# Kernel tuning notes

Measured on AMD Instinct MI355X. Metric: run time of the kernel, lower is better.

## Reference

```python
import jax, jax.numpy as jnp
import numpy as np
import math

D_MODEL = 256


def make_pe(h, w, d):
    # dh channels encode row index, dh channels encode column index,
    # each as interleaved sin/cos with log-spaced frequencies.
    dh = d // 2
    freqs = jnp.exp(jnp.arange(0, dh, 2, dtype=jnp.float32) * (-math.log(10000.0) / dh))  # [dh/2]
    r = jnp.arange(h, dtype=jnp.float32)[:, None] * freqs[None, :]  # [h, dh/2]
    c = jnp.arange(w, dtype=jnp.float32)[:, None] * freqs[None, :]  # [w, dh/2]
    rr = jnp.stack([jnp.sin(r), jnp.cos(r)], axis=-1).reshape(h, dh)  # interleave sin/cos
    cc = jnp.stack([jnp.sin(c), jnp.cos(c)], axis=-1).reshape(w, dh)
    pe = jnp.concatenate([
        jnp.broadcast_to(rr[:, None, :], (h, w, dh)),
        jnp.broadcast_to(cc[None, :, :], (h, w, dh)),
    ], axis=-1)  # [h, w, d]
    return pe.reshape(1, h * w, d)


def setup_inputs() -> dict:
    key = jax.random.key(0)
    h, w = 128, 128
    b = 8
    x = jax.random.normal(key, (b, h * w, D_MODEL), dtype=jnp.float32)
    return {"x": x, "h": h, "w": w}


def reference(x, h, w):
    # Dropout is identity in eval mode; the core op is PE-table generation + add.
    b, l, d = x.shape
    pe = make_pe(h, w, d)  # [1, h*w, d]
    return x + pe[:, :l]
```

## Files before the change

### kernel.cpp

```cpp
#include <hip/hip_runtime.h>
#include <math.h>


typedef float f32x4 __attribute__((ext_vector_type(4)));

__global__ __launch_bounds__(256) void pe_add_kernel(
    const float* __restrict__ x,
    const int* __restrict__ hp,
    const int* __restrict__ wp,
    float* __restrict__ out,
    unsigned int n4)
{
    unsigned int idx = blockIdx.x * blockDim.x + threadIdx.x;
    if (idx >= n4) return;

    const unsigned int ww = (unsigned int)(*wp);
    const unsigned int hh = (unsigned int)(*hp);
    const unsigned int L  = hh * ww;

    const unsigned int j = idx & 63u;
    const unsigned int t = idx >> 6;

    unsigned int l, row, col;
    if (((ww & (ww - 1u)) | (L & (L - 1u))) == 0u) {
        const unsigned int wshift = (unsigned int)__builtin_ctz(ww);
        l   = t & (L - 1u);
        row = l >> wshift;
        col = l & (ww - 1u);
    } else {
        l   = t % L;
        row = l / ww;
        col = l - row * ww;
    }

    const unsigned int d0 = j << 2;
    const unsigned int dd = d0 & 127u;
    const float pos = (float)((d0 < 128u) ? row : col);

    const unsigned int m0 = dd >> 1;
    const float cstep = 0.14391156831212787f;
    const float f0 = __expf(-(float)m0 * cstep);
    const float f1 = __expf(-(float)(m0 + 1u) * cstep);

    float s0, c0, s1, c1;
    __sincosf(pos * f0, &s0, &c0);
    __sincosf(pos * f1, &s1, &c1);

    const f32x4 xv = reinterpret_cast<const f32x4*>(x)[idx];
    const f32x4 pe = { s0, c0, s1, c1 };
    const f32x4 ov = xv + pe;
    __builtin_nontemporal_store(ov, reinterpret_cast<f32x4*>(out) + idx);
}

extern "C" void kernel_launch(void* const* d_in, const int* in_sizes, int n_in,
                              void* d_out, int out_size, void* d_ws, size_t ws_size,
                              hipStream_t stream) {
    const float* x = (const float*)d_in[0];
    const int* hp  = (const int*)d_in[1];
    const int* wp  = (const int*)d_in[2];
    float* out     = (float*)d_out;

    const unsigned int n4 = (unsigned int)(out_size / 4);
    const unsigned int blocks = (n4 + 255u) / 256u;
    pe_add_kernel<<<blocks, 256, 0, stream>>>(x, hp, wp, out, n4);
}
```

Baseline: 226.7 us.

## Precompute PE table in workspace and add via table lookup

Adds a first kernel that writes the positional-encoding table for one batch into workspace. The add kernel then loads table entries instead of computing exp and sincos per element. It falls back to inline computation when the workspace is too small. This trades transcendental math for extra table reads that are likely cache-resident, and it replaces the nontemporal store with a normal store.

```diff
diff --git a/kernel.cpp b/kernel.cpp
--- a/kernel.cpp
+++ b/kernel.cpp
@@ -4,40 +4,18 @@
 
 typedef float f32x4 __attribute__((ext_vector_type(4)));
 
-__global__ __launch_bounds__(256) void pe_add_kernel(
-    const float* __restrict__ x,
-    const int* __restrict__ hp,
-    const int* __restrict__ wp,
-    float* __restrict__ out,
-    unsigned int n4)
+__device__ __forceinline__ f32x4 pe_value(unsigned int l, unsigned int j,
+                                          unsigned int ww, bool wpow2,
+                                          unsigned int wshift)
 {
-    unsigned int idx = blockIdx.x * blockDim.x + threadIdx.x;
-    if (idx >= n4) return;
-
-    const unsigned int ww = (unsigned int)(*wp);
-    const unsigned int hh = (unsigned int)(*hp);
-    const unsigned int L  = hh * ww;
-
-    const unsigned int j = idx & 63u;
-    const unsigned int t = idx >> 6;
-
-    unsigned int l, row, col;
-    if (((ww & (ww - 1u)) | (L & (L - 1u))) == 0u) {
-        const unsigned int wshift = (unsigned int)__builtin_ctz(ww);
-        l   = t & (L - 1u);
-        row = l >> wshift;
-        col = l & (ww - 1u);
-    } else {
-        l   = t % L;
-        row = l / ww;
-        col = l - row * ww;
-    }
+    unsigned int row, col;
+    if (wpow2) { row = l >> wshift; col = l & (ww - 1u); }
+    else       { row = l / ww;      col = l - row * ww; }
 
     const unsigned int d0 = j << 2;
-    const unsigned int dd = d0 & 127u;
+    const unsigned int m0 = (d0 & 127u) >> 1;
     const float pos = (float)((d0 < 128u) ? row : col);
 
-    const unsigned int m0 = dd >> 1;
     const float cstep = 0.14391156831212787f;
     const float f0 = __expf(-(float)m0 * cstep);
     const float f1 = __expf(-(float)(m0 + 1u) * cstep);
@@ -45,11 +23,67 @@
     float s0, c0, s1, c1;
     __sincosf(pos * f0, &s0, &c0);
     __sincosf(pos * f1, &s1, &c1);
+    return (f32x4){ s0, c0, s1, c1 };
+}
+
+__global__ __launch_bounds__(256) void pe_table_kernel(
+    const int* __restrict__ hp,
+    const int* __restrict__ wp,
+    f32x4* __restrict__ tbl,
+    unsigned long long ws_bytes)
+{
+    const unsigned int ww = (unsigned int)(*wp);
+    const unsigned int hh = (unsigned int)(*hp);
+    const unsigned int L  = hh * ww;
+    const unsigned int span = L << 6;
+    if ((unsigned long long)span * 16ull > ws_bytes) return;
+
+    const bool wpow2 = (ww & (ww - 1u)) == 0u;
+    const unsigned int wshift = (unsigned int)__builtin_ctz(ww);
+
+    const unsigned int stride = gridDim.x * blockDim.x;
+    for (unsigned int u = blockIdx.x * blockDim.x + threadIdx.x;
+         u < span; u += stride) {
+        tbl[u] = pe_value(u >> 6, u & 63u, ww, wpow2, wshift);
+    }
+}
+
+__global__ __launch_bounds__(256) void pe_add_table(
+    const float* __restrict__ x,
+    const int* __restrict__ hp,
+    const int* __restrict__ wp,
+    const f32x4* __restrict__ tbl,
+    float* __restrict__ out,
+    unsigned int n4,
+    unsigned long long ws_bytes)
+{
+    const unsigned int idx = blockIdx.x * blockDim.x + threadIdx.x;
+    if (idx >= n4) return;
+
+    const unsigned int ww = (unsigned int)(*wp);
+    const unsigned int hh = (unsigned int)(*hp);
+    const unsigned int L  = hh * ww;
+    const unsigned int span = L << 6;
 
     const f32x4 xv = reinterpret_cast<const f32x4*>(x)[idx];
-    const f32x4 pe = { s0, c0, s1, c1 };
-    const f32x4 ov = xv + pe;
-    __builtin_nontemporal_store(ov, reinterpret_cast<f32x4*>(out) + idx);
+    f32x4 pe;
+
+    if ((unsigned long long)span * 16ull <= ws_bytes) {
+        unsigned int ti;
+        if ((span & (span - 1u)) == 0u) ti = idx & (span - 1u);
+        else                            ti = idx % span;
+        pe = tbl[ti];
+    } else {
+        const bool wpow2 = (ww & (ww - 1u)) == 0u;
+        const unsigned int wshift = (unsigned int)__builtin_ctz(ww);
+        const unsigned int t = idx >> 6;
+        unsigned int l;
+        if ((L & (L - 1u)) == 0u) l = t & (L - 1u);
+        else                      l = t % L;
+        pe = pe_value(l, idx & 63u, ww, wpow2, wshift);
+    }
+
+    reinterpret_cast<f32x4*>(out)[idx] = xv + pe;
 }
 
 extern "C" void kernel_launch(void* const* d_in, const int* in_sizes, int n_in,
@@ -59,8 +93,13 @@
     const int* hp  = (const int*)d_in[1];
     const int* wp  = (const int*)d_in[2];
     float* out     = (float*)d_out;
+    f32x4* tbl     = (f32x4*)d_ws;
 
     const unsigned int n4 = (unsigned int)(out_size / 4);
+    const unsigned long long wsb = (unsigned long long)ws_size;
+
+    pe_table_kernel<<<4096, 256, 0, stream>>>(hp, wp, tbl, wsb);
+
     const unsigned int blocks = (n4 + 255u) / 256u;
-    pe_add_kernel<<<blocks, 256, 0, stream>>>(x, hp, wp, out, n4);
+    pe_add_table<<<blocks, 256, 0, stream>>>(x, hp, wp, tbl, out, n4, wsb);
 }
```

After: 232.6 us. 1.03x slower.
